# Optimization experiments

Hardware: AMD Instinct MI355X
Metric: run time of the kernel (lower is better)

Reference implementation:

```python
import jax, jax.numpy as jnp
import numpy as np
from jax import lax

B, H, L, DK = 8, 8, 1024, 64
BN_EPS = 1e-5


def _conv_bn_sm(x, w, b, g, beta, pad):
    # x: [B, H, L] (N=batch, C=h heads as channels, spatial=L)
    y = lax.conv_general_dilated(x, w, (1,), [(pad, pad)], dimension_numbers=("NCH", "OIH", "NCH"))
    y = y + b[None, :, None]
    # BatchNorm1d in training mode: batch stats over (N, L) per channel, biased var
    mu = jnp.mean(y, axis=(0, 2), keepdims=True)
    var = jnp.var(y, axis=(0, 2), keepdims=True)
    y = (y - mu) * (g[None, :, None] / jnp.sqrt(var + BN_EPS)) + beta[None, :, None]
    return jax.nn.softmax(y, axis=-1)


def setup_inputs() -> dict:
    key = jax.random.key(0)
    ks = jax.random.split(key, 20)
    n = lambda i, shape, s=1.0: jax.random.normal(ks[i], shape, dtype=jnp.float32) * s
    inp = {
        "Q": n(0, (B, H, L, DK)),
        "K": n(1, (B, H, L, DK)),
        "V": n(2, (B, H, L, DK)),
        "attn_mask": jnp.ones((1,), dtype=bool),
        # proj_q / proj_k: Linear(d_k, 1, bias=False) weight [1, d_k] -> stored as [d_k]
        "wq": n(3, (DK,), 0.1), "wk": n(4, (DK,), 0.1),
        # proj_back_q / proj_back_k: Linear(1, d_k, bias=False) weight [d_k, 1] -> [d_k]
        "wbq": n(5, (DK,), 0.1), "wbk": n(6, (DK,), 0.1),
        # Conv1d(h, h, f) weights [out=h, in=h, f] + bias [h]
        "cq3_w": n(7, (H, H, 3), 0.2), "cq3_b": n(8, (H,), 0.05),
        "cq9_w": n(9, (H, H, 9), 0.1), "cq9_b": n(10, (H,), 0.05),
        "ck3_w": n(11, (H, H, 3), 0.2), "ck3_b": n(12, (H,), 0.05),
        "ck9_w": n(13, (H, H, 9), 0.1), "ck9_b": n(14, (H,), 0.05),
        # BatchNorm1d affine params
        "bnq3_g": jnp.ones((H,), jnp.float32), "bnq3_b": jnp.zeros((H,), jnp.float32),
        "bnq9_g": jnp.ones((H,), jnp.float32), "bnq9_b": jnp.zeros((H,), jnp.float32),
        "bnk3_g": jnp.ones((H,), jnp.float32), "bnk3_b": jnp.zeros((H,), jnp.float32),
        "bnk9_g": jnp.ones((H,), jnp.float32), "bnk9_b": jnp.zeros((H,), jnp.float32),
    }
    return inp


def reference(Q, K, V, attn_mask, wq, wk, wbq, wbk,
              cq3_w, cq3_b, cq9_w, cq9_b, ck3_w, ck3_b, ck9_w, ck9_b,
              bnq3_g, bnq3_b, bnq9_g, bnq9_b, bnk3_g, bnk3_b, bnk9_g, bnk9_b):
    b, h, l, d_k = Q.shape
    l_k = K.shape[2]
    # proj to scalar per position, reshape to [b, h, l]
    Qp = jnp.einsum("bhld,d->bhl", Q, wq)
    Kp = jnp.einsum("bhld,d->bhl", K, wk)
    # multi-scale conv + BN(train) + softmax branches
    q0 = _conv_bn_sm(Qp, cq3_w, cq3_b, bnq3_g, bnq3_b, 1)
    q1 = _conv_bn_sm(Qp, cq9_w, cq9_b, bnq9_g, bnq9_b, 4)
    k0 = _conv_bn_sm(Kp, ck3_w, ck3_b, bnk3_g, bnk3_b, 1)
    k1 = _conv_bn_sm(Kp, ck9_w, ck9_b, bnk9_g, bnk9_b, 4)
    # faithful to torch: cat along dim 0 then C-order reshape to [b,h,l,2], max over last
    Qm = jnp.max(jnp.concatenate([q0, q1], axis=0).reshape(b, h, l, 2), axis=-1)
    Km = jnp.max(jnp.concatenate([k0, k1], axis=0).reshape(b, h, l_k, 2), axis=-1)
    # proj back 1 -> d_k (no bias): outer with weight vector
    Qn = Qm[..., None] * wbq  # [b,h,l,d_k]
    Kn = Km[..., None] * wbk  # [b,h,l_k,d_k]
    scores = jnp.einsum("bhqd,bhkd->bhqk", Qn, Kn) / jnp.sqrt(jnp.float32(d_k))
    attn = jax.nn.softmax(scores, axis=-1)
    context = jnp.einsum("bhqk,bhkd->bhqd", attn, V)
    return (context, attn)
```

## Files before the change

kernel.cpp:

```cpp
#include <hip/hip_runtime.h>

constexpr int SL = 1024;
constexpr int NBH = 64;

constexpr int QP_OFF = 0;
constexpr int KP_OFF = 65536;
constexpr int Y_OFF  = 131072;
constexpr int QM_OFF = 655360;
constexpr int KM_OFF = 720896;
constexpr int ST_OFF = 786432;
constexpr int C_OFF  = 786496;
constexpr int VT_OFF = 786560;

typedef __attribute__((ext_vector_type(8))) short short8;
typedef __attribute__((ext_vector_type(4))) float f32x4;

__device__ inline unsigned short f2bf(float x) {
    unsigned int u = __float_as_uint(x);
    unsigned int r = (u + 0x7fff + ((u >> 16) & 1)) >> 16;
    return (unsigned short)r;
}

__global__ __launch_bounds__(256) void k_projpack(
    const float* __restrict__ Q, const float* __restrict__ K,
    const float* __restrict__ V,
    const float* __restrict__ wq, const float* __restrict__ wk,
    const float* __restrict__ wbq, const float* __restrict__ wbk,
    float* __restrict__ ws)
{
    int b = blockIdx.x;
    int tid = threadIdx.x;
    if (b < 8192) {
        bool isQ = b < 4096;
        const float* src = isQ ? Q : K;
        const float* w   = isQ ? wq : wk;
        int row = (b - (isQ ? 0 : 4096)) * 16 + (tid >> 4);
        int l16 = tid & 15;
        float4 x  = ((const float4*)(src + row * 64))[l16];
        float4 w4 = ((const float4*)w)[l16];
        float v = x.x * w4.x + x.y * w4.y + x.z * w4.z + x.w * w4.w;
        #pragma unroll
        for (int m = 8; m; m >>= 1) v += __shfl_xor(v, m);
        if (l16 == 0) ws[(isQ ? QP_OFF : KP_OFF) + row] = v;
    } else if (b < 10240) {
        int t = (b - 8192) * 256 + tid;
        int lane = t & 63;
        int s    = (t >> 6) & 7;
        int dsub = (t >> 9) & 3;
        int chunk= (t >> 11) & 3;
        int bh   = t >> 13;
        const float* vb = V + bh * (SL * 64);
        int k0 = chunk * 256 + s * 32 + (lane >> 4) * 8;
        int d  = dsub * 16 + (lane & 15);
        unsigned short o[8];
        #pragma unroll
        for (int j = 0; j < 8; j++) o[j] = f2bf(vb[(k0 + j) * 64 + d]);
        unsigned short* vt = (unsigned short*)(ws + VT_OFF);
        *(short8*)(vt + (size_t)t * 8) = *(short8*)o;
    } else {
        if (tid < 64) {
            ws[ST_OFF + tid] = 0.f;
            float v = wbq[tid] * wbk[tid];
            #pragma unroll
            for (int m = 32; m; m >>= 1) v += __shfl_xor(v, m);
            if (tid == 0) ws[C_OFF] = v * 0.125f;
        }
    }
}

__global__ __launch_bounds__(256) void k_conv(
    float* __restrict__ ws,
    const float* __restrict__ w0, const float* __restrict__ b0,
    const float* __restrict__ w1, const float* __restrict__ b1,
    const float* __restrict__ w2, const float* __restrict__ b2,
    const float* __restrict__ w3, const float* __restrict__ b3)
{
    int branch = blockIdx.x >> 6;
    int n = (blockIdx.x >> 3) & 7;
    int seg = blockIdx.x & 7;
    int t0 = seg * 128;
    const float* wp = branch == 0 ? w0 : branch == 1 ? w1 : branch == 2 ? w2 : w3;
    const float* bp = branch == 0 ? b0 : branch == 1 ? b1 : branch == 2 ? b2 : b3;
    const int F = (branch & 1) ? 9 : 3;
    const int PAD = F >> 1;
    const float* x = ws + ((branch < 2) ? QP_OFF : KP_OFF) + n * 8 * SL;

    __shared__ float xl[8][136];
    __shared__ float wl[8 * 8 * 9];
    __shared__ float bl[8];
    int tid = threadIdx.x;
    for (int i = tid; i < 8 * 8 * F; i += 256) wl[i] = wp[i];
    if (tid < 8) bl[tid] = bp[tid];
    for (int i = tid; i < 8 * 136; i += 256) {
        int ci = i / 136; int tt = i - ci * 136;
        int ta = t0 + tt - 4;
        xl[ci][tt] = (ta >= 0 && ta < SL) ? x[ci * SL + ta] : 0.f;
    }
    __syncthreads();
    int c = tid >> 5, u = tid & 31;
    float s1 = 0.f, s2 = 0.f;
    float* yout = ws + Y_OFF + branch * (NBH * SL) + (n * 8 + c) * SL + t0;
    #pragma unroll
    for (int q = 0; q < 4; q++) {
        int tl = q * 32 + u;
        float acc = bl[c];
        for (int ci = 0; ci < 8; ci++) {
            const float* xr = &xl[ci][tl + 4 - PAD];
            const float* wr = &wl[(c * 8 + ci) * F];
            for (int f = 0; f < F; f++) acc += wr[f] * xr[f];
        }
        yout[tl] = acc;
        s1 += acc; s2 += acc * acc;
    }
    #pragma unroll
    for (int m = 16; m; m >>= 1) {
        s1 += __shfl_xor(s1, m);
        s2 += __shfl_xor(s2, m);
    }
    if (u == 0) {
        atomicAdd(&ws[ST_OFF + (branch * 8 + c) * 2],     s1);
        atomicAdd(&ws[ST_OFF + (branch * 8 + c) * 2 + 1], s2);
    }
}

__global__ __launch_bounds__(256) void k_bnmix(
    float* __restrict__ ws,
    const float* __restrict__ g0, const float* __restrict__ be0,
    const float* __restrict__ g1, const float* __restrict__ be1,
    const float* __restrict__ g2, const float* __restrict__ be2,
    const float* __restrict__ g3, const float* __restrict__ be3)
{
    int blk = blockIdx.x;
    int which = blk >> 6;
    int i = (blk >> 3) & 7, j = blk & 7;
    int n = 2 * i + (j >= 4 ? 1 : 0);
    int br = which * 2 + (n >= 8 ? 1 : 0);
    int row = n & 7;
    int tid = threadIdx.x;
    int half = tid >> 7;
    int u = tid & 127;
    int c = 2 * (j & 3) + half;
    const float* gp = br == 0 ? g0 : br == 1 ? g1 : br == 2 ? g2 : g3;
    const float* bp = br == 0 ? be0 : br == 1 ? be1 : br == 2 ? be2 : be3;
    float s1 = ws[ST_OFF + (br * 8 + c) * 2];
    float s2 = ws[ST_OFF + (br * 8 + c) * 2 + 1];
    float mu  = s1 * (1.f / 8192.f);
    float var = s2 * (1.f / 8192.f) - mu * mu;
    float sc = gp[c] * rsqrtf(var + 1e-5f);
    float sh = bp[c] - mu * sc;
    const float* y = ws + Y_OFF + br * (NBH * SL) + (row * 8 + c) * SL;
    float4 ya = ((const float4*)y)[u * 2];
    float4 yb = ((const float4*)y)[u * 2 + 1];
    float z[8] = { ya.x * sc + sh, ya.y * sc + sh, ya.z * sc + sh, ya.w * sc + sh,
                   yb.x * sc + sh, yb.y * sc + sh, yb.z * sc + sh, yb.w * sc + sh };
    float mx = z[0];
    #pragma unroll
    for (int q = 1; q < 8; q++) mx = fmaxf(mx, z[q]);
    __shared__ float r1[4], r2[4];
    #pragma unroll
    for (int m = 32; m; m >>= 1) mx = fmaxf(mx, __shfl_xor(mx, m));
    if ((tid & 63) == 0) r1[tid >> 6] = mx;
    __syncthreads();
    mx = half ? fmaxf(r1[2], r1[3]) : fmaxf(r1[0], r1[1]);
    float e[8];
    float s = 0.f;
    #pragma unroll
    for (int q = 0; q < 8; q++) { e[q] = __expf(z[q] - mx); s += e[q]; }
    #pragma unroll
    for (int m = 32; m; m >>= 1) s += __shfl_xor(s, m);
    if ((tid & 63) == 0) r2[tid >> 6] = s;
    __syncthreads();
    s = half ? (r2[2] + r2[3]) : (r2[0] + r2[1]);
    float inv = 1.f / s;
    float4 o = make_float4(fmaxf(e[0], e[1]) * inv, fmaxf(e[2], e[3]) * inv,
                           fmaxf(e[4], e[5]) * inv, fmaxf(e[6], e[7]) * inv);
    float* outp = ws + (which ? KM_OFF : QM_OFF) + i * 8192 + j * 1024 + half * 512;
    ((float4*)outp)[u] = o;
}

__global__ __launch_bounds__(256, 3) void k_attn(
    float* __restrict__ out, const float* __restrict__ ws)
{
    int p = blockIdx.x;
    int xcd = p & 7, idx = p >> 3;
    int bh = xcd + 8 * (idx >> 4);
    int qc = idx & 15;
    int tid = threadIdx.x;

    __shared__ __align__(16) float kml[1024];
    __shared__ float rmx[4], rmn[4];
    __shared__ float wsum[4][16];
    __shared__ float accred[4][16][64];

    const float* km = ws + KM_OFF + bh * SL;
    const float* qm = ws + QM_OFF + bh * SL + qc * 64;
    float c = ws[C_OFF];

    float lmax = -1e30f, lmin = 1e30f;
    #pragma unroll
    for (int i = 0; i < 4; i++) {
        float v = km[tid + 256 * i];
        kml[tid + 256 * i] = v;
        lmax = fmaxf(lmax, v); lmin = fminf(lmin, v);
    }
    #pragma unroll
    for (int m = 32; m; m >>= 1) {
        lmax = fmaxf(lmax, __shfl_xor(lmax, m));
        lmin = fminf(lmin, __shfl_xor(lmin, m));
    }
    if ((tid & 63) == 0) { rmx[tid >> 6] = lmax; rmn[tid >> 6] = lmin; }
    __syncthreads();
    float kmax = fmaxf(fmaxf(rmx[0], rmx[1]), fmaxf(rmx[2], rmx[3]));
    float kmin = fminf(fminf(rmn[0], rmn[1]), fminf(rmn[2], rmn[3]));

    int w = tid >> 6, lane = tid & 63;
    int m16 = lane & 15, kg = lane >> 4;
    const short8* vt8 = (const short8*)((const unsigned short*)(ws + VT_OFF))
                        + (size_t)bh * 8192 + w * 2048;

    for (int t = 0; t < 4; ++t) {
        float a = c * qm[t * 16 + m16];
        float mm = (a > 0.f) ? a * kmax : a * kmin;

        float e[64];
        float rowsum = 0.f;
        #pragma unroll
        for (int s = 0; s < 8; s++) {
            const float4* kp = (const float4*)(kml + w * 256 + s * 32 + kg * 8);
            float4 ka = kp[0], kb = kp[1];
            e[s * 8 + 0] = __expf(a * ka.x - mm);
            e[s * 8 + 1] = __expf(a * ka.y - mm);
            e[s * 8 + 2] = __expf(a * ka.z - mm);
            e[s * 8 + 3] = __expf(a * ka.w - mm);
            e[s * 8 + 4] = __expf(a * kb.x - mm);
            e[s * 8 + 5] = __expf(a * kb.y - mm);
            e[s * 8 + 6] = __expf(a * kb.z - mm);
            e[s * 8 + 7] = __expf(a * kb.w - mm);
            #pragma unroll
            for (int j = 0; j < 8; j++) rowsum += e[s * 8 + j];
        }
        rowsum += __shfl_xor(rowsum, 16);
        rowsum += __shfl_xor(rowsum, 32);
        if (lane < 16) wsum[w][lane] = rowsum;
        __syncthreads();
        float rr = 1.f / (wsum[0][m16] + wsum[1][m16] + wsum[2][m16] + wsum[3][m16]);

        float* attn_row = out + 4194304
                        + ((size_t)(bh * SL + qc * 64 + t * 16 + m16)) * SL;

        f32x4 acc0 = {0,0,0,0}, acc1 = {0,0,0,0}, acc2 = {0,0,0,0}, acc3 = {0,0,0,0};

        #pragma unroll
        for (int s = 0; s < 8; s++) {
            int k0 = w * 256 + s * 32 + kg * 8;
            float es[8];
            #pragma unroll
            for (int j = 0; j < 8; j++) es[j] = e[s * 8 + j] * rr;
            *(float4*)(attn_row + k0)     = make_float4(es[0], es[1], es[2], es[3]);
            *(float4*)(attn_row + k0 + 4) = make_float4(es[4], es[5], es[6], es[7]);
            unsigned short af[8];
            #pragma unroll
            for (int j = 0; j < 8; j++) af[j] = f2bf(es[j]);
            short8 av = *(short8*)af;
            const short8* bbase = vt8 + s * 64 + lane;
            short8 b0 = bbase[0 * 512];
            short8 b1 = bbase[1 * 512];
            short8 b2 = bbase[2 * 512];
            short8 b3 = bbase[3 * 512];
            acc0 = __builtin_amdgcn_mfma_f32_16x16x32_bf16(av, b0, acc0, 0, 0, 0);
            acc1 = __builtin_amdgcn_mfma_f32_16x16x32_bf16(av, b1, acc1, 0, 0, 0);
            acc2 = __builtin_amdgcn_mfma_f32_16x16x32_bf16(av, b2, acc2, 0, 0, 0);
            acc3 = __builtin_amdgcn_mfma_f32_16x16x32_bf16(av, b3, acc3, 0, 0, 0);
        }

        #pragma unroll
        for (int reg = 0; reg < 4; reg++) {
            int r = kg * 4 + reg;
            accred[w][r][ 0 + m16] = acc0[reg];
            accred[w][r][16 + m16] = acc1[reg];
            accred[w][r][32 + m16] = acc2[reg];
            accred[w][r][48 + m16] = acc3[reg];
        }
        __syncthreads();
        {
            int r  = tid >> 4;
            int d0 = (tid & 15) * 4;
            float4 s0 = *(const float4*)&accred[0][r][d0];
            float4 s1 = *(const float4*)&accred[1][r][d0];
            float4 s2 = *(const float4*)&accred[2][r][d0];
            float4 s3 = *(const float4*)&accred[3][r][d0];
            float4 o = make_float4(s0.x + s1.x + s2.x + s3.x,
                                   s0.y + s1.y + s2.y + s3.y,
                                   s0.z + s1.z + s2.z + s3.z,
                                   s0.w + s1.w + s2.w + s3.w);
            float* ctx = out + ((size_t)(bh * SL + qc * 64 + t * 16 + r)) * 64 + d0;
            *(float4*)ctx = o;
        }
        __syncthreads();
    }
}

extern "C" void kernel_launch(void* const* d_in, const int* in_sizes, int n_in,
                              void* d_out, int out_size, void* d_ws, size_t ws_size,
                              hipStream_t stream)
{
    const float* Q      = (const float*)d_in[0];
    const float* K      = (const float*)d_in[1];
    const float* V      = (const float*)d_in[2];
    const float* wq     = (const float*)d_in[4];
    const float* wk     = (const float*)d_in[5];
    const float* wbq    = (const float*)d_in[6];
    const float* wbk    = (const float*)d_in[7];
    const float* cq3_w  = (const float*)d_in[8];
    const float* cq3_b  = (const float*)d_in[9];
    const float* cq9_w  = (const float*)d_in[10];
    const float* cq9_b  = (const float*)d_in[11];
    const float* ck3_w  = (const float*)d_in[12];
    const float* ck3_b  = (const float*)d_in[13];
    const float* ck9_w  = (const float*)d_in[14];
    const float* ck9_b  = (const float*)d_in[15];
    const float* bnq3_g = (const float*)d_in[16];
    const float* bnq3_b = (const float*)d_in[17];
    const float* bnq9_g = (const float*)d_in[18];
    const float* bnq9_b = (const float*)d_in[19];
    const float* bnk3_g = (const float*)d_in[20];
    const float* bnk3_b = (const float*)d_in[21];
    const float* bnk9_g = (const float*)d_in[22];
    const float* bnk9_b = (const float*)d_in[23];
    float* out = (float*)d_out;
    float* ws  = (float*)d_ws;

    k_projpack<<<10241, 256, 0, stream>>>(Q, K, V, wq, wk, wbq, wbk, ws);
    k_conv<<<256, 256, 0, stream>>>(ws, cq3_w, cq3_b, cq9_w, cq9_b,
                                    ck3_w, ck3_b, ck9_w, ck9_b);
    k_bnmix<<<128, 256, 0, stream>>>(ws, bnq3_g, bnq3_b, bnq9_g, bnq9_b,
                                     bnk3_g, bnk3_b, bnk9_g, bnk9_b);
    k_attn<<<1024, 256, 0, stream>>>(out, ws);
}
```

Baseline: 465.4 us.

## Restructure attention kernel to two interleaved query tiles per block, recompute exps

Each attention block now handles 32 query rows (two 16-row tiles processed together) instead of looping over four 16-row tiles, and the grid doubles to 2048 blocks. The 64-element exp array is no longer held in registers; exponentials are computed once for the row sums and again in the output pass, and the V fragments are loaded once and shared by both tiles' MFMAs. Launch bounds rise to 4 blocks per SIMD to raise occupancy. This trades doubled exp work for lower register pressure, more parallelism and less V reloading, with more K reloading per block.

Measured after the change: 393.3 us, median of 2. 15.5% less time.

```diff
diff --git a/kernel.cpp b/kernel.cpp
--- a/kernel.cpp
+++ b/kernel.cpp
@@ -178,22 +178,22 @@
     ((float4*)outp)[u] = o;
 }
 
-__global__ __launch_bounds__(256, 3) void k_attn(
+__global__ __launch_bounds__(256, 4) void k_attn(
     float* __restrict__ out, const float* __restrict__ ws)
 {
     int p = blockIdx.x;
     int xcd = p & 7, idx = p >> 3;
-    int bh = xcd + 8 * (idx >> 4);
-    int qc = idx & 15;
+    int bh = xcd + 8 * (idx >> 5);
+    int qt2 = idx & 31;
     int tid = threadIdx.x;
 
     __shared__ __align__(16) float kml[1024];
     __shared__ float rmx[4], rmn[4];
-    __shared__ float wsum[4][16];
+    __shared__ float wsum0[4][16], wsum1[4][16];
     __shared__ float accred[4][16][64];
 
     const float* km = ws + KM_OFF + bh * SL;
-    const float* qm = ws + QM_OFF + bh * SL + qc * 64;
+    const float* qm = ws + QM_OFF + bh * SL + qt2 * 32;
     float c = ws[C_OFF];
 
     float lmax = -1e30f, lmin = 1e30f;
@@ -210,93 +210,145 @@
     }
     if ((tid & 63) == 0) { rmx[tid >> 6] = lmax; rmn[tid >> 6] = lmin; }
     __syncthreads();
+
+    int w = tid >> 6, lane = tid & 63;
+    int m16 = lane & 15, kg = lane >> 4;
     float kmax = fmaxf(fmaxf(rmx[0], rmx[1]), fmaxf(rmx[2], rmx[3]));
     float kmin = fminf(fminf(rmn[0], rmn[1]), fminf(rmn[2], rmn[3]));
-
-    int w = tid >> 6, lane = tid & 63;
-    int m16 = lane & 15, kg = lane >> 4;
+    float a0 = c * qm[m16];
+    float a1 = c * qm[16 + m16];
+    float mm0 = (a0 > 0.f) ? a0 * kmax : a0 * kmin;
+    float mm1 = (a1 > 0.f) ? a1 * kmax : a1 * kmin;
+
+    float rs0 = 0.f, rs1 = 0.f;
+    #pragma unroll
+    for (int s = 0; s < 8; s++) {
+        const float4* kp = (const float4*)(kml + w * 256 + s * 32 + kg * 8);
+        float4 ka = kp[0], kb = kp[1];
+        rs0 += __expf(a0 * ka.x - mm0); rs1 += __expf(a1 * ka.x - mm1);
+        rs0 += __expf(a0 * ka.y - mm0); rs1 += __expf(a1 * ka.y - mm1);
+        rs0 += __expf(a0 * ka.z - mm0); rs1 += __expf(a1 * ka.z - mm1);
+        rs0 += __expf(a0 * ka.w - mm0); rs1 += __expf(a1 * ka.w - mm1);
+        rs0 += __expf(a0 * kb.x - mm0); rs1 += __expf(a1 * kb.x - mm1);
+        rs0 += __expf(a0 * kb.y - mm0); rs1 += __expf(a1 * kb.y - mm1);
+        rs0 += __expf(a0 * kb.z - mm0); rs1 += __expf(a1 * kb.z - mm1);
+        rs0 += __expf(a0 * kb.w - mm0); rs1 += __expf(a1 * kb.w - mm1);
+    }
+    rs0 += __shfl_xor(rs0, 16); rs0 += __shfl_xor(rs0, 32);
+    rs1 += __shfl_xor(rs1, 16); rs1 += __shfl_xor(rs1, 32);
+    if (lane < 16) { wsum0[w][lane] = rs0; wsum1[w][lane] = rs1; }
+    __syncthreads();
+    float rr0 = 1.f / (wsum0[0][m16] + wsum0[1][m16] + wsum0[2][m16] + wsum0[3][m16]);
+    float rr1 = 1.f / (wsum1[0][m16] + wsum1[1][m16] + wsum1[2][m16] + wsum1[3][m16]);
+
+    float* attn_row0 = out + 4194304 + ((size_t)(bh * SL + qt2 * 32 + m16)) * SL;
+    float* attn_row1 = attn_row0 + (size_t)16 * SL;
     const short8* vt8 = (const short8*)((const unsigned short*)(ws + VT_OFF))
                         + (size_t)bh * 8192 + w * 2048;
 
-    for (int t = 0; t < 4; ++t) {
-        float a = c * qm[t * 16 + m16];
-        float mm = (a > 0.f) ? a * kmax : a * kmin;
-
-        float e[64];
-        float rowsum = 0.f;
-        #pragma unroll
-        for (int s = 0; s < 8; s++) {
-            const float4* kp = (const float4*)(kml + w * 256 + s * 32 + kg * 8);
-            float4 ka = kp[0], kb = kp[1];
-            e[s * 8 + 0] = __expf(a * ka.x - mm);
-            e[s * 8 + 1] = __expf(a * ka.y - mm);
-            e[s * 8 + 2] = __expf(a * ka.z - mm);
-            e[s * 8 + 3] = __expf(a * ka.w - mm);
-            e[s * 8 + 4] = __expf(a * kb.x - mm);
-            e[s * 8 + 5] = __expf(a * kb.y - mm);
-            e[s * 8 + 6] = __expf(a * kb.z - mm);
-            e[s * 8 + 7] = __expf(a * kb.w - mm);
-            #pragma unroll
-            for (int j = 0; j < 8; j++) rowsum += e[s * 8 + j];
-        }
-        rowsum += __shfl_xor(rowsum, 16);
-        rowsum += __shfl_xor(rowsum, 32);
-        if (lane < 16) wsum[w][lane] = rowsum;
-        __syncthreads();
-        float rr = 1.f / (wsum[0][m16] + wsum[1][m16] + wsum[2][m16] + wsum[3][m16]);
-
-        float* attn_row = out + 4194304
-                        + ((size_t)(bh * SL + qc * 64 + t * 16 + m16)) * SL;
-
-        f32x4 acc0 = {0,0,0,0}, acc1 = {0,0,0,0}, acc2 = {0,0,0,0}, acc3 = {0,0,0,0};
-
-        #pragma unroll
-        for (int s = 0; s < 8; s++) {
-            int k0 = w * 256 + s * 32 + kg * 8;
+    f32x4 p0a = {0,0,0,0}, p0b = {0,0,0,0}, p0c = {0,0,0,0}, p0d = {0,0,0,0};
+    f32x4 p1a = {0,0,0,0}, p1b = {0,0,0,0}, p1c = {0,0,0,0}, p1d = {0,0,0,0};
+
+    #pragma unroll
+    for (int s = 0; s < 8; s++) {
+        int k0 = w * 256 + s * 32 + kg * 8;
+        const float4* kp = (const float4*)(kml + k0);
+        float4 ka = kp[0], kb = kp[1];
+        const short8* bbase = vt8 + s * 64 + lane;
+        short8 b0 = bbase[0 * 512];
+        short8 b1 = bbase[1 * 512];
+        short8 b2 = bbase[2 * 512];
+        short8 b3 = bbase[3 * 512];
+        {
             float es[8];
-            #pragma unroll
-            for (int j = 0; j < 8; j++) es[j] = e[s * 8 + j] * rr;
-            *(float4*)(attn_row + k0)     = make_float4(es[0], es[1], es[2], es[3]);
-            *(float4*)(attn_row + k0 + 4) = make_float4(es[4], es[5], es[6], es[7]);
+            es[0] = __expf(a0 * ka.x - mm0) * rr0;
+            es[1] = __expf(a0 * ka.y - mm0) * rr0;
+            es[2] = __expf(a0 * ka.z - mm0) * rr0;
+            es[3] = __expf(a0 * ka.w - mm0) * rr0;
+            es[4] = __expf(a0 * kb.x - mm0) * rr0;
+            es[5] = __expf(a0 * kb.y - mm0) * rr0;
+            es[6] = __expf(a0 * kb.z - mm0) * rr0;
+            es[7] = __expf(a0 * kb.w - mm0) * rr0;
+            *(float4*)(attn_row0 + k0)     = make_float4(es[0], es[1], es[2], es[3]);
+            *(float4*)(attn_row0 + k0 + 4) = make_float4(es[4], es[5], es[6], es[7]);
             unsigned short af[8];
             #pragma unroll
             for (int j = 0; j < 8; j++) af[j] = f2bf(es[j]);
             short8 av = *(short8*)af;
-            const short8* bbase = vt8 + s * 64 + lane;
-            short8 b0 = bbase[0 * 512];
-            short8 b1 = bbase[1 * 512];
-            short8 b2 = bbase[2 * 512];
-            short8 b3 = bbase[3 * 512];
-            acc0 = __builtin_amdgcn_mfma_f32_16x16x32_bf16(av, b0, acc0, 0, 0, 0);
-            acc1 = __builtin_amdgcn_mfma_f32_16x16x32_bf16(av, b1, acc1, 0, 0, 0);
-            acc2 = __builtin_amdgcn_mfma_f32_16x16x32_bf16(av, b2, acc2, 0, 0, 0);
-            acc3 = __builtin_amdgcn_mfma_f32_16x16x32_bf16(av, b3, acc3, 0, 0, 0);
+            p0a = __builtin_amdgcn_mfma_f32_16x16x32_bf16(av, b0, p0a, 0, 0, 0);
+            p0b = __builtin_amdgcn_mfma_f32_16x16x32_bf16(av, b1, p0b, 0, 0, 0);
+            p0c = __builtin_amdgcn_mfma_f32_16x16x32_bf16(av, b2, p0c, 0, 0, 0);
+            p0d = __builtin_amdgcn_mfma_f32_16x16x32_bf16(av, b3, p0d, 0, 0, 0);
         }
-
-        #pragma unroll
-        for (int reg = 0; reg < 4; reg++) {
-            int r = kg * 4 + reg;
-            accred[w][r][ 0 + m16] = acc0[reg];
-            accred[w][r][16 + m16] = acc1[reg];
-            accred[w][r][32 + m16] = acc2[reg];
-            accred[w][r][48 + m16] = acc3[reg];
+        {
+            float es[8];
+            es[0] = __expf(a1 * ka.x - mm1) * rr1;
+            es[1] = __expf(a1 * ka.y - mm1) * rr1;
+            es[2] = __expf(a1 * ka.z - mm1) * rr1;
+            es[3] = __expf(a1 * ka.w - mm1) * rr1;
+            es[4] = __expf(a1 * kb.x - mm1) * rr1;
+            es[5] = __expf(a1 * kb.y - mm1) * rr1;
+            es[6] = __expf(a1 * kb.z - mm1) * rr1;
+            es[7] = __expf(a1 * kb.w - mm1) * rr1;
+            *(float4*)(attn_row1 + k0)     = make_float4(es[0], es[1], es[2], es[3]);
+            *(float4*)(attn_row1 + k0 + 4) = make_float4(es[4], es[5], es[6], es[7]);
+            unsigned short af[8];
+            #pragma unroll
+            for (int j = 0; j < 8; j++) af[j] = f2bf(es[j]);
+            short8 av = *(short8*)af;
+            p1a = __builtin_amdgcn_mfma_f32_16x16x32_bf16(av, b0, p1a, 0, 0, 0);
+            p1b = __builtin_amdgcn_mfma_f32_16x16x32_bf16(av, b1, p1b, 0, 0, 0);
+            p1c = __builtin_amdgcn_mfma_f32_16x16x32_bf16(av, b2, p1c, 0, 0, 0);
+            p1d = __builtin_amdgcn_mfma_f32_16x16x32_bf16(av, b3, p1d, 0, 0, 0);
         }
-        __syncthreads();
-        {
-            int r  = tid >> 4;
-            int d0 = (tid & 15) * 4;
-            float4 s0 = *(const float4*)&accred[0][r][d0];
-            float4 s1 = *(const float4*)&accred[1][r][d0];
-            float4 s2 = *(const float4*)&accred[2][r][d0];
-            float4 s3 = *(const float4*)&accred[3][r][d0];
-            float4 o = make_float4(s0.x + s1.x + s2.x + s3.x,
-                                   s0.y + s1.y + s2.y + s3.y,
-                                   s0.z + s1.z + s2.z + s3.z,
-                                   s0.w + s1.w + s2.w + s3.w);
-            float* ctx = out + ((size_t)(bh * SL + qc * 64 + t * 16 + r)) * 64 + d0;
-            *(float4*)ctx = o;
-        }
-        __syncthreads();
+    }
+
+    #pragma unroll
+    for (int reg = 0; reg < 4; reg++) {
+        int r = kg * 4 + reg;
+        accred[w][r][ 0 + m16] = p0a[reg];
+        accred[w][r][16 + m16] = p0b[reg];
+        accred[w][r][32 + m16] = p0c[reg];
+        accred[w][r][48 + m16] = p0d[reg];
+    }
+    __syncthreads();
+    {
+        int r  = tid >> 4;
+        int d0 = (tid & 15) * 4;
+        float4 s0 = *(const float4*)&accred[0][r][d0];
+        float4 s1 = *(const float4*)&accred[1][r][d0];
+        float4 s2 = *(const float4*)&accred[2][r][d0];
+        float4 s3 = *(const float4*)&accred[3][r][d0];
+        float4 o = make_float4(s0.x + s1.x + s2.x + s3.x,
+                               s0.y + s1.y + s2.y + s3.y,
+                               s0.z + s1.z + s2.z + s3.z,
+                               s0.w + s1.w + s2.w + s3.w);
+        float* ctx = out + ((size_t)(bh * SL + qt2 * 32 + r)) * 64 + d0;
+        *(float4*)ctx = o;
+    }
+    __syncthreads();
+    #pragma unroll
+    for (int reg = 0; reg < 4; reg++) {
+        int r = kg * 4 + reg;
+        accred[w][r][ 0 + m16] = p1a[reg];
+        accred[w][r][16 + m16] = p1b[reg];
+        accred[w][r][32 + m16] = p1c[reg];
+        accred[w][r][48 + m16] = p1d[reg];
+    }
+    __syncthreads();
+    {
+        int r  = tid >> 4;
+        int d0 = (tid & 15) * 4;
+        float4 s0 = *(const float4*)&accred[0][r][d0];
+        float4 s1 = *(const float4*)&accred[1][r][d0];
+        float4 s2 = *(const float4*)&accred[2][r][d0];
+        float4 s3 = *(const float4*)&accred[3][r][d0];
+        float4 o = make_float4(s0.x + s1.x + s2.x + s3.x,
+                               s0.y + s1.y + s2.y + s3.y,
+                               s0.z + s1.z + s2.z + s3.z,
+                               s0.w + s1.w + s2.w + s3.w);
+        float* ctx = out + ((size_t)(bh * SL + qt2 * 32 + 16 + r)) * 64 + d0;
+        *(float4*)ctx = o;
     }
 }
 
@@ -335,5 +387,5 @@
                                     ck3_w, ck3_b, ck9_w, ck9_b);
     k_bnmix<<<128, 256, 0, stream>>>(ws, bnq3_g, bnq3_b, bnq9_g, bnq9_b,
                                      bnk3_g, bnk3_b, bnk9_g, bnk9_b);
-    k_attn<<<1024, 256, 0, stream>>>(out, ws);
-}
+    k_attn<<<2048, 256, 0, stream>>>(out, ws);
+}
```
